# Kernel tuning notes

Measured on AMD Instinct MI355X. Metric: run time of the kernel, lower is better.

## Reference

```python
import jax, jax.numpy as jnp
import numpy as np

NUM_SEGMENTS = 4096  # number of graphs in the batch


def setup_inputs() -> dict:
    key = jax.random.key(0)
    k1, k2, k3, k4, k5, k6 = jax.random.split(key, 6)
    N, H = 1048576, 128
    x = jax.random.normal(k1, (N, H), dtype=jnp.float32)
    batch = jnp.sort(jax.random.randint(k2, (N,), 0, NUM_SEGMENTS, dtype=jnp.int64))
    # Linear params, PyTorch layout: W [out, in], b [out]
    W1 = jax.random.normal(k3, (2 * H, H), dtype=jnp.float32) * (1.0 / np.sqrt(H))
    b1 = jax.random.normal(k4, (2 * H,), dtype=jnp.float32) * 0.01
    W2 = jax.random.normal(k5, (H, 2 * H), dtype=jnp.float32) * (1.0 / np.sqrt(2 * H))
    b2 = jax.random.normal(k6, (H,), dtype=jnp.float32) * 0.01
    return {"x": x, "batch": batch, "W1": W1, "b1": b1, "W2": W2, "b2": b2}


def reference(x, batch, W1, b1, W2, b2):
    # phi(x) = tanh(fc1(x))  -> [N, 2H]
    phi_x = jnp.tanh(jnp.einsum('nh,oh->no', x, W1) + b1)
    # scatter-sum pooling per graph -> [G, 2H]
    sum_x = jax.ops.segment_sum(phi_x, batch, num_segments=NUM_SEGMENTS)
    # fc2 -> [G, H]; .squeeze() is a no-op for these shapes
    y = jnp.einsum('go,ho->gh', sum_x, W2) + b2
    return jnp.squeeze(y)
```

## Files before the change

kernel.cpp:

```cpp
#include <hip/hip_runtime.h>
#include <hip/hip_bf16.h>

#define NTOT 1048576
#define NSEG 4096
#define HDIM 128
#define ODIM 256
#define GRID1 2048
#define NSTEP 8
#define PSEG 8

typedef __attribute__((ext_vector_type(8))) short bf16x8;
typedef __attribute__((ext_vector_type(4))) float f32x4;
typedef __attribute__((ext_vector_type(4))) unsigned int u32x4;

__device__ __forceinline__ unsigned int cvt_pk(float lo, float hi) {
    unsigned int r;
    asm("v_cvt_pk_bf16_f32 %0, %1, %2" : "=v"(r) : "v"(lo), "v"(hi));
    return r;
}

__global__ void zero_convert(const float* __restrict__ W1, unsigned int* __restrict__ W1b,
                             float* __restrict__ sumx) {
    int gid = blockIdx.x * 256 + threadIdx.x;
    sumx[gid] = 0.0f;
    if (gid < (ODIM * HDIM / 2)) {
        float2 v = *(const float2*)(W1 + 2 * gid);
        W1b[gid] = cvt_pk(v.x, v.y);
    }
}

__global__ __launch_bounds__(256, 2)
void stage1(const float* __restrict__ x, const int* __restrict__ batch,
            const unsigned short* __restrict__ W1b, const float* __restrict__ b1,
            float* __restrict__ sumx) {
    __shared__ __align__(16) unsigned char w1s[ODIM * HDIM * 2];
    __shared__ float part[PSEG * ODIM];
    __shared__ int segAll[512];

    const int t    = threadIdx.x;
    const int lane = t & 63;
    const int wv   = t >> 6;
    const int l15  = lane & 15;
    const int lhi  = (lane >> 4) & 3;

    const bool is64 = (batch[NTOT - 1] == 0);
    const long blockrow = (long)blockIdx.x * 512;

    for (int c = t; c < 4096; c += 256) {
        u32x4 v = ((const u32x4*)W1b)[c];
        int row = c >> 4;
        int kb  = (c & 15) * 16;
        *(u32x4*)(w1s + row * 256 + (kb ^ ((row & 7) << 4))) = v;
    }
    for (int i = t; i < 512; i += 256) {
        long idx = blockrow + i;
        segAll[i] = batch[is64 ? 2 * idx : idx];
    }
    for (int i = t; i < PSEG * ODIM; i += 256) part[i] = 0.f;

    float bias[16];
    #pragma unroll
    for (int nf = 0; nf < 16; ++nf) bias[nf] = b1[nf * 16 + l15];

    const int segBase = batch[is64 ? 2 * blockrow : blockrow];

    __syncthreads();

    int lra[4];
    #pragma unroll
    for (int ks = 0; ks < 4; ++ks)
        lra[ks] = l15 * 256 + ((ks * 64 + lhi * 16) ^ ((l15 & 7) << 4));

    const long rowbase = blockrow + (long)wv * 128;
    const char* xrow = (const char*)x + (rowbase + l15) * 512 + lhi * 32;

    int curSeg = segAll[wv * 128];
    float runsum[16];
    #pragma unroll
    for (int nf = 0; nf < 16; ++nf) runsum[nf] = 0.f;

#define LOADSTEP(dst, s)                                                             \
    do { const float* _b = (const float*)(xrow + (size_t)(s) * 8192);                \
        asm volatile("global_load_dwordx4 %0, %1, off"            : "=v"(dst[0]) : "v"(_b)); \
        asm volatile("global_load_dwordx4 %0, %1, off offset:16"  : "=v"(dst[1]) : "v"(_b)); \
        asm volatile("global_load_dwordx4 %0, %1, off offset:128" : "=v"(dst[2]) : "v"(_b)); \
        asm volatile("global_load_dwordx4 %0, %1, off offset:144" : "=v"(dst[3]) : "v"(_b)); \
        asm volatile("global_load_dwordx4 %0, %1, off offset:256" : "=v"(dst[4]) : "v"(_b)); \
        asm volatile("global_load_dwordx4 %0, %1, off offset:272" : "=v"(dst[5]) : "v"(_b)); \
        asm volatile("global_load_dwordx4 %0, %1, off offset:384" : "=v"(dst[6]) : "v"(_b)); \
        asm volatile("global_load_dwordx4 %0, %1, off offset:400" : "=v"(dst[7]) : "v"(_b)); \
    } while (0)

#define FLUSH()                                                                   \
    do { if (lhi == 0) {                                                          \
            const unsigned _idx = (unsigned)(curSeg - segBase);                   \
            if (_idx < PSEG) {                                                    \
                float* _p = &part[_idx * ODIM + l15];                             \
                _Pragma("unroll")                                                 \
                for (int nf = 0; nf < 16; ++nf)                                   \
                    atomicAdd(_p + nf * 16, runsum[nf]);          \
            } else {                                                              \
                float* _b = sumx + (long)curSeg * ODIM + l15;                     \
                _Pragma("unroll")                                                 \
                for (int nf = 0; nf < 16; ++nf)                                   \
                    atomicAdd(_b + nf * 16, runsum[nf]);                          \
                                \
                asm volatile("s_waitcnt vmcnt(0)" ::: "memory");                  \
                __builtin_amdgcn_sched_barrier(0);                                \
            }                                                                     \
        }                                                                         \
        _Pragma("unroll")                                                         \
        for (int nf = 0; nf < 16; ++nf) runsum[nf] = 0.f;                         \
    } while (0)

#define STEP(s, cur, nxt)                                                         \
    do {                                                                          \
        if ((s) + 1 < NSTEP) {                                                    \
            LOADSTEP(nxt, (s) + 1);                                               \
            asm volatile("s_waitcnt vmcnt(8)" ::: "memory");     \
        } else {                                                                  \
            asm volatile("s_waitcnt vmcnt(0)" ::: "memory");                      \
        }                                                                         \
        __builtin_amdgcn_sched_barrier(0);                           \
        int seg_l = segAll[wv * 128 + (s) * 16 + l15];           \
        int prv   = __shfl(seg_l, lane > 0 ? lane - 1 : 0);                       \
        unsigned bm = (unsigned)(__ballot(seg_l != prv)) & 0xFFFEu;               \
        int seg0 = __shfl(seg_l, 0);                                              \
        f32x4 acc[16];                                                            \
        _Pragma("unroll")                                                         \
        for (int nf = 0; nf < 16; ++nf)                                           \
            acc[nf] = (f32x4){bias[nf], bias[nf], bias[nf], bias[nf]};            \
        _Pragma("unroll")                                                         \
        for (int ks = 0; ks < 4; ++ks) {                                          \
            u32x4 w;                                                              \
            w.x = cvt_pk(cur[2*ks].x,   cur[2*ks].y);                             \
            w.y = cvt_pk(cur[2*ks].z,   cur[2*ks].w);                             \
            w.z = cvt_pk(cur[2*ks+1].x, cur[2*ks+1].y);                           \
            w.w = cvt_pk(cur[2*ks+1].z, cur[2*ks+1].w);                           \
            bf16x8 af = __builtin_bit_cast(bf16x8, w);                            \
            _Pragma("unroll")                                                     \
            for (int nf = 0; nf < 16; ++nf) {                                     \
                bf16x8 bf = *(const bf16x8*)(w1s + lra[ks] + nf * 4096);          \
                acc[nf] = __builtin_amdgcn_mfma_f32_16x16x32_bf16(af, bf, acc[nf], 0, 0, 0); \
            }                                                                     \
        }                                                                         \
        _Pragma("unroll")                                                         \
        for (int nf = 0; nf < 16; ++nf)                                           \
            _Pragma("unroll")                                                     \
            for (int r = 0; r < 4; ++r) {                                         \
                float e = exp2f(acc[nf][r] * 2.885390081777927f);                 \
                acc[nf][r] = 1.0f - 2.0f * __builtin_amdgcn_rcpf(1.0f + e);       \
            }                                                                     \
        if (seg0 != curSeg) { FLUSH(); curSeg = seg0; }                           \
        int start = 0;                                                            \
        unsigned rem = bm;                                                        \
        for (;;) {                                                                \
            const int end = rem ? (int)__builtin_ctz(rem) : 16;                   \
            _Pragma("unroll")                                                     \
            for (int nf = 0; nf < 16; ++nf) {                                     \
                float sp = 0.f;                                                   \
                _Pragma("unroll")                                                 \
                for (int r = 0; r < 4; ++r) {                                     \
                    int row = lhi * 4 + r;                                        \
                    float wgt = ((unsigned)(row - start) < (unsigned)(end - start)) ? 1.0f : 0.0f; \
                    sp = fmaf(wgt, acc[nf][r], sp);                               \
                }                                                                 \
                sp += __shfl_xor(sp, 16);                                         \
                sp += __shfl_xor(sp, 32);                                         \
                runsum[nf] += sp;                                                 \
            }                                                                     \
            if (end == 16) break;                                                 \
            FLUSH();                                                              \
            curSeg = __shfl(seg_l, end);                                          \
            rem &= rem - 1;                                                       \
            start = end;                                                          \
        }                                                                         \
    } while (0)

    f32x4 cA[8], cB[8];
    LOADSTEP(cA, 0);
    #pragma unroll
    for (int s = 0; s < NSTEP; s += 2) {
        STEP(s, cA, cB);
        STEP(s + 1, cB, cA);
    }
    FLUSH();

#undef STEP
#undef FLUSH
#undef LOADSTEP

    __syncthreads();
    const int segLast = segAll[511];
    int nrows = segLast - segBase + 1;
    if (nrows > PSEG) nrows = PSEG;
    for (int i = t; i < nrows * ODIM; i += 256)
        atomicAdd(&sumx[(long)(segBase + (i >> 8)) * ODIM + (i & 255)], part[i]);
}

__global__ __launch_bounds__(256)
void stage2(const float* __restrict__ sumx, const float* __restrict__ W2,
            const float* __restrict__ b2, float* __restrict__ y) {
    __shared__ float sx[16 * 256];
    const int t = threadIdx.x;
    const long g0 = (long)blockIdx.x * 16;
    #pragma unroll
    for (int i = 0; i < 16; ++i)
        sx[i * 256 + t] = sumx[(g0 + i) * 256 + t];
    __syncthreads();
    const int h = t & 127;
    const int gl0 = (t >> 7) * 8;
    float acc[8] = {0, 0, 0, 0, 0, 0, 0, 0};
    const float* w = W2 + h * 256;
    for (int o4 = 0; o4 < 64; ++o4) {
        float4 wvv = *(const float4*)(w + o4 * 4);
        #pragma unroll
        for (int gl = 0; gl < 8; ++gl) {
            const float* sr = &sx[(gl0 + gl) * 256 + o4 * 4];
            acc[gl] += sr[0] * wvv.x + sr[1] * wvv.y + sr[2] * wvv.z + sr[3] * wvv.w;
        }
    }
    float bb = b2[h];
    #pragma unroll
    for (int gl = 0; gl < 8; ++gl)
        y[(g0 + gl0 + gl) * 128 + h] = acc[gl] + bb;
}

extern "C" void kernel_launch(void* const* d_in, const int* in_sizes, int n_in,
                              void* d_out, int out_size, void* d_ws, size_t ws_size,
                              hipStream_t stream) {
    const float* x   = (const float*)d_in[0];
    const int* batch = (const int*)d_in[1];
    const float* W1  = (const float*)d_in[2];
    const float* b1  = (const float*)d_in[3];
    const float* W2  = (const float*)d_in[4];
    const float* b2  = (const float*)d_in[5];
    float* y = (float*)d_out;

    float* sumx = (float*)d_ws;
    unsigned short* W1b = (unsigned short*)((char*)d_ws + (size_t)NSEG * ODIM * 4);

    zero_convert<<<dim3(NSEG), dim3(256), 0, stream>>>(W1, (unsigned int*)W1b, sumx);
    stage1<<<dim3(GRID1), dim3(256), 0, stream>>>(x, batch, W1b, b1, sumx);
    stage2<<<dim3(NSEG / 16), dim3(256), 0, stream>>>(sumx, W2, b2, y);
}
```

Baseline: 244.7 us.

## Split output columns across waves and keep W1 fragments in registers

Each block now handles 128 rows, with its four waves splitting the 256 output columns (64 each) instead of splitting rows. Each wave holds its W1 bf16 fragments in registers, which removes the 64KB shared-memory staging of W1 and the per-MFMA LDS reads. Every wave now loads the same x rows, so global/L2 traffic for x rises up to fourfold. The grid grows to 8192 blocks to cover the rows.

```diff
diff --git a/kernel.cpp b/kernel.cpp
--- a/kernel.cpp
+++ b/kernel.cpp
@@ -5,7 +5,7 @@
 #define NSEG 4096
 #define HDIM 128
 #define ODIM 256
-#define GRID1 2048
+#define GRID1 8192
 #define NSTEP 8
 #define PSEG 8
 
@@ -33,51 +33,42 @@
 void stage1(const float* __restrict__ x, const int* __restrict__ batch,
             const unsigned short* __restrict__ W1b, const float* __restrict__ b1,
             float* __restrict__ sumx) {
-    __shared__ __align__(16) unsigned char w1s[ODIM * HDIM * 2];
     __shared__ float part[PSEG * ODIM];
-    __shared__ int segAll[512];
+    __shared__ int segAll[128];
 
     const int t    = threadIdx.x;
     const int lane = t & 63;
     const int wv   = t >> 6;
     const int l15  = lane & 15;
     const int lhi  = (lane >> 4) & 3;
+    const int cb   = wv * 64;
 
     const bool is64 = (batch[NTOT - 1] == 0);
-    const long blockrow = (long)blockIdx.x * 512;
-
-    for (int c = t; c < 4096; c += 256) {
-        u32x4 v = ((const u32x4*)W1b)[c];
-        int row = c >> 4;
-        int kb  = (c & 15) * 16;
-        *(u32x4*)(w1s + row * 256 + (kb ^ ((row & 7) << 4))) = v;
-    }
-    for (int i = t; i < 512; i += 256) {
-        long idx = blockrow + i;
-        segAll[i] = batch[is64 ? 2 * idx : idx];
+    const long blockrow = (long)blockIdx.x * 128;
+
+    if (t < 128) {
+        long idx = blockrow + t;
+        segAll[t] = batch[is64 ? 2 * idx : idx];
     }
     for (int i = t; i < PSEG * ODIM; i += 256) part[i] = 0.f;
 
-    float bias[16];
-    #pragma unroll
-    for (int nf = 0; nf < 16; ++nf) bias[nf] = b1[nf * 16 + l15];
-
+    bf16x8 bfr[4][4];
+    #pragma unroll
+    for (int nf = 0; nf < 4; ++nf)
+        #pragma unroll
+        for (int ks = 0; ks < 4; ++ks)
+            bfr[nf][ks] = *(const bf16x8*)(W1b + (cb + nf * 16 + l15) * HDIM + ks * 32 + lhi * 8);
+    float bias[4];
+    #pragma unroll
+    for (int nf = 0; nf < 4; ++nf) bias[nf] = b1[cb + nf * 16 + l15];
     const int segBase = batch[is64 ? 2 * blockrow : blockrow];
 
     __syncthreads();
 
-    int lra[4];
-    #pragma unroll
-    for (int ks = 0; ks < 4; ++ks)
-        lra[ks] = l15 * 256 + ((ks * 64 + lhi * 16) ^ ((l15 & 7) << 4));
-
-    const long rowbase = blockrow + (long)wv * 128;
-    const char* xrow = (const char*)x + (rowbase + l15) * 512 + lhi * 32;
-
-    int curSeg = segAll[wv * 128];
-    float runsum[16];
-    #pragma unroll
-    for (int nf = 0; nf < 16; ++nf) runsum[nf] = 0.f;
+    const char* xrow = (const char*)x + (blockrow + l15) * 512 + lhi * 32;
+
+    int curSeg = segAll[0];
+    float runsum[4] = {0.f, 0.f, 0.f, 0.f};
 
 #define LOADSTEP(dst, s)                                                             \
     do { const float* _b = (const float*)(xrow + (size_t)(s) * 8192);                \
@@ -95,22 +86,21 @@
     do { if (lhi == 0) {                                                          \
             const unsigned _idx = (unsigned)(curSeg - segBase);                   \
             if (_idx < PSEG) {                                                    \
-                float* _p = &part[_idx * ODIM + l15];                             \
+                float* _p = &part[_idx * ODIM + cb + l15];                        \
                 _Pragma("unroll")                                                 \
-                for (int nf = 0; nf < 16; ++nf)                                   \
+                for (int nf = 0; nf < 4; ++nf)                                    \
                     atomicAdd(_p + nf * 16, runsum[nf]);          \
-            } else {                                                              \
-                float* _b = sumx + (long)curSeg * ODIM + l15;                     \
+            } else {                                                 \
+                float* _b = sumx + (long)curSeg * ODIM + cb + l15;                \
                 _Pragma("unroll")                                                 \
-                for (int nf = 0; nf < 16; ++nf)                                   \
+                for (int nf = 0; nf < 4; ++nf)                                    \
                     atomicAdd(_b + nf * 16, runsum[nf]);                          \
-                                \
-                asm volatile("s_waitcnt vmcnt(0)" ::: "memory");                  \
+                asm volatile("s_waitcnt vmcnt(0)" ::: "memory");    \
                 __builtin_amdgcn_sched_barrier(0);                                \
             }                                                                     \
         }                                                                         \
         _Pragma("unroll")                                                         \
-        for (int nf = 0; nf < 16; ++nf) runsum[nf] = 0.f;                         \
+        for (int nf = 0; nf < 4; ++nf) runsum[nf] = 0.f;                          \
     } while (0)
 
 #define STEP(s, cur, nxt)                                                         \
@@ -122,13 +112,13 @@
             asm volatile("s_waitcnt vmcnt(0)" ::: "memory");                      \
         }                                                                         \
         __builtin_amdgcn_sched_barrier(0);                           \
-        int seg_l = segAll[wv * 128 + (s) * 16 + l15];           \
+        int seg_l = segAll[(s) * 16 + l15];                      \
         int prv   = __shfl(seg_l, lane > 0 ? lane - 1 : 0);                       \
         unsigned bm = (unsigned)(__ballot(seg_l != prv)) & 0xFFFEu;               \
         int seg0 = __shfl(seg_l, 0);                                              \
-        f32x4 acc[16];                                                            \
-        _Pragma("unroll")                                                         \
-        for (int nf = 0; nf < 16; ++nf)                                           \
+        f32x4 acc[4];                                                             \
+        _Pragma("unroll")                                                         \
+        for (int nf = 0; nf < 4; ++nf)                                            \
             acc[nf] = (f32x4){bias[nf], bias[nf], bias[nf], bias[nf]};            \
         _Pragma("unroll")                                                         \
         for (int ks = 0; ks < 4; ++ks) {                                          \
@@ -139,13 +129,11 @@
             w.w = cvt_pk(cur[2*ks+1].z, cur[2*ks+1].w);                           \
             bf16x8 af = __builtin_bit_cast(bf16x8, w);                            \
             _Pragma("unroll")                                                     \
-            for (int nf = 0; nf < 16; ++nf) {                                     \
-                bf16x8 bf = *(const bf16x8*)(w1s + lra[ks] + nf * 4096);          \
-                acc[nf] = __builtin_amdgcn_mfma_f32_16x16x32_bf16(af, bf, acc[nf], 0, 0, 0); \
-            }                                                                     \
-        }                                                                         \
-        _Pragma("unroll")                                                         \
-        for (int nf = 0; nf < 16; ++nf)                                           \
+            for (int nf = 0; nf < 4; ++nf)                                        \
+                acc[nf] = __builtin_amdgcn_mfma_f32_16x16x32_bf16(af, bfr[nf][ks], acc[nf], 0, 0, 0); \
+        }                                                                         \
+        _Pragma("unroll")                                                         \
+        for (int nf = 0; nf < 4; ++nf)                                            \
             _Pragma("unroll")                                                     \
             for (int r = 0; r < 4; ++r) {                                         \
                 float e = exp2f(acc[nf][r] * 2.885390081777927f);                 \
@@ -157,7 +145,7 @@
         for (;;) {                                                                \
             const int end = rem ? (int)__builtin_ctz(rem) : 16;                   \
             _Pragma("unroll")                                                     \
-            for (int nf = 0; nf < 16; ++nf) {                                     \
+            for (int nf = 0; nf < 4; ++nf) {                                      \
                 float sp = 0.f;                                                   \
                 _Pragma("unroll")                                                 \
                 for (int r = 0; r < 4; ++r) {                                     \
@@ -191,7 +179,7 @@
 #undef LOADSTEP
 
     __syncthreads();
-    const int segLast = segAll[511];
+    const int segLast = segAll[127];
     int nrows = segLast - segBase + 1;
     if (nrows > PSEG) nrows = PSEG;
     for (int i = t; i < nrows * ODIM; i += 256)
```

Result: slower. 324.3 us (+32.5%).
